# Kernel optimization log

Measured on AMD Instinct MI355X. Metric: run time of the kernel, lower is better.

## Reference

```python
import jax, jax.numpy as jnp
import numpy as np

T = 8192   # sequence length (= max_seq_len)
E = 1024   # embedding dim
D = 11     # hard-coded projection dim in source


def setup_inputs() -> dict:
    key = jax.random.key(0)
    ks = jax.random.split(key, 6)
    s_e = 1.0 / np.sqrt(E)
    s_d = 1.0 / np.sqrt(D)
    return {
        "x": jax.random.randint(ks[0], (T,), 0, 32000, dtype=jnp.int64),
        "x_embeddings": jax.random.normal(ks[1], (T, E), dtype=jnp.float32),
        "Wk": jax.random.normal(ks[2], (D, E), dtype=jnp.float32) * s_e,
        "bk": jnp.zeros((D,), dtype=jnp.float32),
        "Wq": jax.random.normal(ks[3], (D, E), dtype=jnp.float32) * s_e,
        "bq": jnp.zeros((D,), dtype=jnp.float32),
        "Wv": jax.random.normal(ks[4], (D, E), dtype=jnp.float32) * s_e,
        "bv": jnp.zeros((D,), dtype=jnp.float32),
        "Wf": jax.random.normal(ks[5], (E, D), dtype=jnp.float32) * s_d,
        "bf": jnp.zeros((E,), dtype=jnp.float32),
    }


def reference(x, x_embeddings, Wk, bk, Wq, bq, Wv, bv, Wf, bf):
    t = x.shape[0]  # static under jit
    k = x_embeddings @ Wk.T + bk            # [T, D]
    q = x_embeddings @ Wq.T + bq            # [T, D]
    v = x_embeddings @ Wv.T + bv            # [T, D]
    att = q @ k.T                           # [T, T]; NOTE: no 1/sqrt(D) scaling in source
    causal = jnp.tril(jnp.ones((t, t), dtype=bool))
    att = jnp.where(causal, att, -jnp.inf)
    att = jax.nn.softmax(att, axis=1)       # dim=1 as in source
    res = att @ v                           # [T, D]
    return res @ Wf.T + bf                  # [T, E]
```

## Files before the change

### kernel.cpp

```cpp
#include <hip/hip_runtime.h>

#define T_SEQ 8192
#define E_DIM 1024
#define QS 36
#define QNEC 16
#define QKC 64
#define QX4 16
#define QXST 17
#define QRB 64
#define AJC 64
#define ARB 128
#define KVW 24
#define NSLOT 128
#define TR 16

__device__ __forceinline__ float2 pkfma(float2 a, float2 b, float2 c) {
    return make_float2(fmaf(a.x, b.x, c.x), fmaf(a.y, b.y, c.y));
}
__device__ __forceinline__ float2 f2(float x, float y) { return make_float2(x, y); }


__global__ __launch_bounds__(256) void qkv_proj(
    const float* __restrict__ xe,
    const float* __restrict__ Wk, const float* __restrict__ bk,
    const float* __restrict__ Wq, const float* __restrict__ bq,
    const float* __restrict__ Wv, const float* __restrict__ bv,
    float* __restrict__ partQ) {
    const int row0 = blockIdx.x * QRB;
    const int ec = blockIdx.y;
    const int lane = threadIdx.x & 63;
    const int wg = threadIdx.x >> 6;
    const int cb = ec * QKC;

    __shared__ float4 xT[QRB * QXST];
    __shared__ float4 wT[36 * QX4];

#pragma unroll
    for (int t = 0; t < 4; ++t) {
        int idx = threadIdx.x + t * 256;
        int r = idx >> 4, c4 = idx & 15;
        xT[r * QXST + c4] =
            *(const float4*)(xe + (size_t)(row0 + r) * E_DIM + cb + c4 * 4);
    }
    for (int idx = threadIdx.x; idx < 36 * QX4; idx += 256) {
        int r = idx >> 4, c4 = idx & 15;
        float4 v = make_float4(0.f, 0.f, 0.f, 0.f);
        if (r < 33) {
            const float* base = (r < 11) ? (Wk + (size_t)r * E_DIM)
                              : (r < 22) ? (Wq + (size_t)(r - 11) * E_DIM)
                                         : (Wv + (size_t)(r - 22) * E_DIM);
            v = *(const float4*)(base + cb + c4 * 4);
        }
        wT[idx] = v;
    }
    __syncthreads();

    float2 acc[9];
#pragma unroll
    for (int k = 0; k < 9; ++k) acc[k] = f2(0.f, 0.f);

    const float4* xr = xT + lane * QXST;
    const float4* wr = wT + wg * 9 * QX4;
#pragma unroll 4
    for (int c4 = 0; c4 < QX4; ++c4) {
        float4 xv = xr[c4];
#pragma unroll
        for (int k = 0; k < 9; ++k) {
            float4 wv = wr[k * QX4 + c4];
            acc[k] = pkfma(f2(xv.x, xv.y), f2(wv.x, wv.y), acc[k]);
            acc[k] = pkfma(f2(xv.z, xv.w), f2(wv.z, wv.w), acc[k]);
        }
    }

    __syncthreads();
    float* res = (float*)xT;
#pragma unroll
    for (int k = 0; k < 9; ++k) {
        int o = wg * 9 + k;
        bool live = (o < 33);
        int c = (o < 11) ? o : (o < 22) ? o + 1 : (o < 33) ? o + 2
              : (o == 33) ? 11 : (o == 34) ? 23 : 35;
        float b = 0.f;
        if (ec == 0 && live)
            b = (o < 11) ? bk[o] : (o < 22) ? bq[o - 11] : bv[o - 22];
        res[lane * 36 + c] = live ? (acc[k].x + acc[k].y + b) : 0.f;
    }
    __syncthreads();

    float4* dst = (float4*)(partQ + ((size_t)ec * T_SEQ + row0) * QS);
    for (int idx = threadIdx.x; idx < QRB * 9; idx += 256) {
        int r = idx / 9, f = idx % 9;
        dst[idx] = *(const float4*)(res + r * 36 + f * 4);
    }
}

__global__ __launch_bounds__(256) void reduceQ(const float* __restrict__ partQ,
                                               float* __restrict__ qkvF) {
    const size_t idx = (size_t)blockIdx.x * 256 + threadIdx.x;
    const float4* p = (const float4*)partQ;
    const size_t cs = (size_t)T_SEQ * (QS / 4);
    float4 s = make_float4(0.f, 0.f, 0.f, 0.f);
#pragma unroll
    for (int c = 0; c < QNEC; ++c) {
        float4 a = p[idx + (size_t)c * cs];
        s.x += a.x; s.y += a.y; s.z += a.z; s.w += a.w;
    }
    ((float4*)qkvF)[idx] = s;
}

__global__ __launch_bounds__(128) void attn(const float* __restrict__ qkvF,
                                            float* __restrict__ part) {
    const int b = blockIdx.x;
    int rb = 0;
    while ((rb + 1) * (rb + 2) / 2 <= b) ++rb;
    const int p = b - rb * (rb + 1) / 2;
    const int lane = threadIdx.x & 63;
    const int wid = threadIdx.x >> 6;
    const int jc = 2 * p + wid;
    const int r0 = rb * ARB + lane * 2;
    const int j0 = jc * AJC;

    const float* qp0 = qkvF + (size_t)r0 * QS + 12;
    const float* qp1 = qp0 + QS;
    float2 qa[6], qb[6];
#pragma unroll
    for (int d = 0; d < 5; ++d) {
        qa[d] = f2(qp0[2 * d], qp0[2 * d + 1]);
        qb[d] = f2(qp1[2 * d], qp1[2 * d + 1]);
    }
    qa[5] = f2(qp0[10], 0.f);
    qb[5] = f2(qp1[10], 0.f);

    float2 oa[6], ob[6];
#pragma unroll
    for (int d = 0; d < 6; ++d) { oa[d] = f2(0.f, 0.f); ob[d] = f2(0.f, 0.f); }

    __shared__ float kvs[2][AJC * KVW];
    float* kv = kvs[wid];

#pragma unroll
    for (int t = 0; t < 6; ++t) {
        int idx = lane + t * 64;
        int row = idx / 6, f = idx % 6;
        int srcOff = f * 4 + (f >= 3 ? 12 : 0);
        float4 v = *(const float4*)(qkvF + (size_t)(j0 + row) * QS + srcOff);
        *(float4*)(kv + row * KVW + f * 4) = v;
    }
    __syncthreads();

    for (int jj = 0; jj < AJC; ++jj) {
        const float* kp = kv + jj * KVW;
        const float4 kA = *(const float4*)(kp);
        const float4 kB = *(const float4*)(kp + 4);
        const float4 kC = *(const float4*)(kp + 8);
        const float4 vA = *(const float4*)(kp + 12);
        const float4 vB = *(const float4*)(kp + 16);
        const float4 vC = *(const float4*)(kp + 20);
        const float2 k01 = f2(kA.x, kA.y), k23 = f2(kA.z, kA.w);
        const float2 k45 = f2(kB.x, kB.y), k67 = f2(kB.z, kB.w);
        const float2 k89 = f2(kC.x, kC.y), kXp = f2(kC.z, kC.w);

        float2 sa = pkfma(qa[0], k01, pkfma(qa[1], k23, pkfma(qa[2], k45,
                    pkfma(qa[3], k67, pkfma(qa[4], k89,
                    pkfma(qa[5], kXp, f2(0.f, 0.f)))))));
        float2 sb = pkfma(qb[0], k01, pkfma(qb[1], k23, pkfma(qb[2], k45,
                    pkfma(qb[3], k67, pkfma(qb[4], k89,
                    pkfma(qb[5], kXp, f2(0.f, 0.f)))))));
        float pa = __expf(sa.x + sa.y);
        float pb = __expf(sb.x + sb.y);
        const int j = j0 + jj;
        pa = (j <= r0)     ? pa : 0.f;
        pb = (j <= r0 + 1) ? pb : 0.f;
        float2 pa2 = f2(pa, pa), pb2 = f2(pb, pb);
        oa[0] = pkfma(pa2, f2(vA.x, vA.y), oa[0]);
        oa[1] = pkfma(pa2, f2(vA.z, vA.w), oa[1]);
        oa[2] = pkfma(pa2, f2(vB.x, vB.y), oa[2]);
        oa[3] = pkfma(pa2, f2(vB.z, vB.w), oa[3]);
        oa[4] = pkfma(pa2, f2(vC.x, vC.y), oa[4]);
        oa[5] = pkfma(pa2, f2(vC.z, 1.f),  oa[5]);
        ob[0] = pkfma(pb2, f2(vA.x, vA.y), ob[0]);
        ob[1] = pkfma(pb2, f2(vA.z, vA.w), ob[1]);
        ob[2] = pkfma(pb2, f2(vB.x, vB.y), ob[2]);
        ob[3] = pkfma(pb2, f2(vB.z, vB.w), ob[3]);
        ob[4] = pkfma(pb2, f2(vC.x, vC.y), ob[4]);
        ob[5] = pkfma(pb2, f2(vC.z, 1.f),  ob[5]);
    }

    float* d0 = part + ((size_t)jc * T_SEQ + r0) * 12;
    float4 t;
    t.x = oa[0].x; t.y = oa[0].y; t.z = oa[1].x; t.w = oa[1].y; *(float4*)(d0 + 0) = t;
    t.x = oa[2].x; t.y = oa[2].y; t.z = oa[3].x; t.w = oa[3].y; *(float4*)(d0 + 4) = t;
    t.x = oa[4].x; t.y = oa[4].y; t.z = oa[5].x; t.w = oa[5].y; *(float4*)(d0 + 8) = t;
    float* d1 = d0 + 12;
    t.x = ob[0].x; t.y = ob[0].y; t.z = ob[1].x; t.w = ob[1].y; *(float4*)(d1 + 0) = t;
    t.x = ob[2].x; t.y = ob[2].y; t.z = ob[3].x; t.w = ob[3].y; *(float4*)(d1 + 4) = t;
    t.x = ob[4].x; t.y = ob[4].y; t.z = ob[5].x; t.w = ob[5].y; *(float4*)(d1 + 8) = t;
}

__global__ __launch_bounds__(256) void pass2(const float* __restrict__ part,
                                             const float* __restrict__ Wf,
                                             const float* __restrict__ bf,
                                             float* __restrict__ out) {
    const int t0 = blockIdx.x * TR;
    __shared__ float res[TR][12];
    const int cnt = 2 * (t0 / ARB) + 2;
    if (threadIdx.x < TR * 12) {
        const float* p = part + (size_t)t0 * 12 + threadIdx.x;
        const size_t S = (size_t)T_SEQ * 12;
        float v[4];
#pragma unroll
        for (int u = 0; u < 4; ++u) v[u] = 0.f;
        int c = 0;
        for (; c + 4 <= cnt; c += 4) {
#pragma unroll
            for (int u = 0; u < 4; ++u) v[u] += p[(size_t)(c + u) * S];
        }
        for (; c < cnt; ++c) v[0] += p[(size_t)c * S];
        float sum = (v[0] + v[1]) + (v[2] + v[3]);
        const int d = threadIdx.x % 12;
        res[threadIdx.x / 12][d] = (d == 11) ? (1.f / sum) : sum;
    }
    __syncthreads();

    const int e0 = threadIdx.x * 4;
    float w[4][11];
    const float* wp = Wf + (size_t)e0 * 11;
#pragma unroll
    for (int ee = 0; ee < 4; ++ee)
#pragma unroll
        for (int i = 0; i < 11; ++i) w[ee][i] = wp[ee * 11 + i];
    const float4 bv = *(const float4*)(bf + e0);

    for (int r = 0; r < TR; ++r) {
        float rr[12];
#pragma unroll
        for (int d = 0; d < 12; ++d) rr[d] = res[r][d];
        float2 a0 = f2(0.f, 0.f), a1 = a0, a2 = a0, a3 = a0;
#pragma unroll
        for (int d = 0; d < 10; d += 2) {
            float2 rv = f2(rr[d], rr[d + 1]);
            a0 = pkfma(rv, f2(w[0][d], w[0][d + 1]), a0);
            a1 = pkfma(rv, f2(w[1][d], w[1][d + 1]), a1);
            a2 = pkfma(rv, f2(w[2][d], w[2][d + 1]), a2);
            a3 = pkfma(rv, f2(w[3][d], w[3][d + 1]), a3);
        }
        const float rl = rr[11];
        float4 ov;
        ov.x = (a0.x + a0.y + rr[10] * w[0][10]) * rl + bv.x;
        ov.y = (a1.x + a1.y + rr[10] * w[1][10]) * rl + bv.y;
        ov.z = (a2.x + a2.y + rr[10] * w[2][10]) * rl + bv.z;
        ov.w = (a3.x + a3.y + rr[10] * w[3][10]) * rl + bv.w;
        *(float4*)(out + (size_t)(t0 + r) * E_DIM + e0) = ov;
    }
}

extern "C" void kernel_launch(void* const* d_in, const int* in_sizes, int n_in,
                              void* d_out, int out_size, void* d_ws, size_t ws_size,
                              hipStream_t stream) {
    const float* xe = (const float*)d_in[1];
    const float* Wk = (const float*)d_in[2];
    const float* bk = (const float*)d_in[3];
    const float* Wq = (const float*)d_in[4];
    const float* bq = (const float*)d_in[5];
    const float* Wv = (const float*)d_in[6];
    const float* bv = (const float*)d_in[7];
    const float* Wf = (const float*)d_in[8];
    const float* bf = (const float*)d_in[9];
    float* out = (float*)d_out;

    float* qkvF  = (float*)d_ws;
    float* partQ = qkvF + (size_t)T_SEQ * QS;
    float* part  = partQ;

    qkv_proj<<<dim3(T_SEQ / QRB, QNEC), 256, 0, stream>>>(xe, Wk, bk, Wq, bq, Wv, bv, partQ);
    reduceQ<<<(T_SEQ * (QS / 4)) / 256, 256, 0, stream>>>(partQ, qkvF);
    const int nrb = T_SEQ / ARB;
    attn<<<nrb * (nrb + 1) / 2, 128, 0, stream>>>(qkvF, part);
    pass2<<<T_SEQ / TR, 256, 0, stream>>>(part, Wf, bf, out);
}
```

Baseline: 176.6 us.

## Raise attention register tile to four rows per lane and cut projection splits

The attention kernel now gives each lane four query rows instead of two, so every K/V row loaded from shared memory is reused across more rows. Row blocks double to 256 and the triangular block mapping is updated to match. The QKV projection loops over four E chunks per block, which cuts the split count from 16 to 4 and shrinks the partial-sum traffic that reduceQ reads. pass2 now reduces partials with 16 threads per row using float4 loads and a shared-memory tree. In exchange the attention kernel uses more registers and launches fewer, larger blocks.

```diff
diff --git a/kernel.cpp b/kernel.cpp
--- a/kernel.cpp
+++ b/kernel.cpp
@@ -3,13 +3,13 @@
 #define T_SEQ 8192
 #define E_DIM 1024
 #define QS 36
-#define QNEC 16
+#define QNEC 4
 #define QKC 64
 #define QX4 16
 #define QXST 17
 #define QRB 64
 #define AJC 64
-#define ARB 128
+#define ARB 256
 #define KVW 24
 #define NSLOT 128
 #define TR 16
@@ -30,45 +30,49 @@
     const int ec = blockIdx.y;
     const int lane = threadIdx.x & 63;
     const int wg = threadIdx.x >> 6;
-    const int cb = ec * QKC;
 
     __shared__ float4 xT[QRB * QXST];
     __shared__ float4 wT[36 * QX4];
 
-#pragma unroll
-    for (int t = 0; t < 4; ++t) {
-        int idx = threadIdx.x + t * 256;
-        int r = idx >> 4, c4 = idx & 15;
-        xT[r * QXST + c4] =
-            *(const float4*)(xe + (size_t)(row0 + r) * E_DIM + cb + c4 * 4);
-    }
-    for (int idx = threadIdx.x; idx < 36 * QX4; idx += 256) {
-        int r = idx >> 4, c4 = idx & 15;
-        float4 v = make_float4(0.f, 0.f, 0.f, 0.f);
-        if (r < 33) {
-            const float* base = (r < 11) ? (Wk + (size_t)r * E_DIM)
-                              : (r < 22) ? (Wq + (size_t)(r - 11) * E_DIM)
-                                         : (Wv + (size_t)(r - 22) * E_DIM);
-            v = *(const float4*)(base + cb + c4 * 4);
-        }
-        wT[idx] = v;
-    }
-    __syncthreads();
-
     float2 acc[9];
 #pragma unroll
     for (int k = 0; k < 9; ++k) acc[k] = f2(0.f, 0.f);
 
-    const float4* xr = xT + lane * QXST;
-    const float4* wr = wT + wg * 9 * QX4;
+    for (int cc = 0; cc < 4; ++cc) {
+        const int cb = ec * 256 + cc * QKC;
+        if (cc) __syncthreads();
+
+#pragma unroll
+        for (int t = 0; t < 4; ++t) {
+            int idx = threadIdx.x + t * 256;
+            int r = idx >> 4, c4 = idx & 15;
+            xT[r * QXST + c4] =
+                *(const float4*)(xe + (size_t)(row0 + r) * E_DIM + cb + c4 * 4);
+        }
+        for (int idx = threadIdx.x; idx < 36 * QX4; idx += 256) {
+            int r = idx >> 4, c4 = idx & 15;
+            float4 v = make_float4(0.f, 0.f, 0.f, 0.f);
+            if (r < 33) {
+                const float* base = (r < 11) ? (Wk + (size_t)r * E_DIM)
+                                  : (r < 22) ? (Wq + (size_t)(r - 11) * E_DIM)
+                                             : (Wv + (size_t)(r - 22) * E_DIM);
+                v = *(const float4*)(base + cb + c4 * 4);
+            }
+            wT[idx] = v;
+        }
+        __syncthreads();
+
+        const float4* xr = xT + lane * QXST;
+        const float4* wr = wT + wg * 9 * QX4;
 #pragma unroll 4
-    for (int c4 = 0; c4 < QX4; ++c4) {
-        float4 xv = xr[c4];
-#pragma unroll
-        for (int k = 0; k < 9; ++k) {
-            float4 wv = wr[k * QX4 + c4];
-            acc[k] = pkfma(f2(xv.x, xv.y), f2(wv.x, wv.y), acc[k]);
-            acc[k] = pkfma(f2(xv.z, xv.w), f2(wv.z, wv.w), acc[k]);
+        for (int c4 = 0; c4 < QX4; ++c4) {
+            float4 xv = xr[c4];
+#pragma unroll
+            for (int k = 0; k < 9; ++k) {
+                float4 wv = wr[k * QX4 + c4];
+                acc[k] = pkfma(f2(xv.x, xv.y), f2(wv.x, wv.y), acc[k]);
+                acc[k] = pkfma(f2(xv.z, xv.w), f2(wv.z, wv.w), acc[k]);
+            }
         }
     }
 
@@ -112,28 +116,24 @@
                                             float* __restrict__ part) {
     const int b = blockIdx.x;
     int rb = 0;
-    while ((rb + 1) * (rb + 2) / 2 <= b) ++rb;
-    const int p = b - rb * (rb + 1) / 2;
+    while ((rb + 1) * (rb + 2) <= b) ++rb;
+    const int p = b - rb * (rb + 1);
     const int lane = threadIdx.x & 63;
     const int wid = threadIdx.x >> 6;
     const int jc = 2 * p + wid;
-    const int r0 = rb * ARB + lane * 2;
+    const int r0 = rb * ARB + lane * 4;
     const int j0 = jc * AJC;
 
-    const float* qp0 = qkvF + (size_t)r0 * QS + 12;
-    const float* qp1 = qp0 + QS;
-    float2 qa[6], qb[6];
-#pragma unroll
-    for (int d = 0; d < 5; ++d) {
-        qa[d] = f2(qp0[2 * d], qp0[2 * d + 1]);
-        qb[d] = f2(qp1[2 * d], qp1[2 * d + 1]);
-    }
-    qa[5] = f2(qp0[10], 0.f);
-    qb[5] = f2(qp1[10], 0.f);
-
-    float2 oa[6], ob[6];
-#pragma unroll
-    for (int d = 0; d < 6; ++d) { oa[d] = f2(0.f, 0.f); ob[d] = f2(0.f, 0.f); }
+    float2 q[4][6], o[4][6];
+#pragma unroll
+    for (int i = 0; i < 4; ++i) {
+        const float* qp = qkvF + (size_t)(r0 + i) * QS + 12;
+#pragma unroll
+        for (int d = 0; d < 5; ++d) q[i][d] = f2(qp[2 * d], qp[2 * d + 1]);
+        q[i][5] = f2(qp[10], 0.f);
+#pragma unroll
+        for (int d = 0; d < 6; ++d) o[i][d] = f2(0.f, 0.f);
+    }
 
     __shared__ float kvs[2][AJC * KVW];
     float* kv = kvs[wid];
@@ -159,42 +159,36 @@
         const float2 k01 = f2(kA.x, kA.y), k23 = f2(kA.z, kA.w);
         const float2 k45 = f2(kB.x, kB.y), k67 = f2(kB.z, kB.w);
         const float2 k89 = f2(kC.x, kC.y), kXp = f2(kC.z, kC.w);
-
-        float2 sa = pkfma(qa[0], k01, pkfma(qa[1], k23, pkfma(qa[2], k45,
-                    pkfma(qa[3], k67, pkfma(qa[4], k89,
-                    pkfma(qa[5], kXp, f2(0.f, 0.f)))))));
-        float2 sb = pkfma(qb[0], k01, pkfma(qb[1], k23, pkfma(qb[2], k45,
-                    pkfma(qb[3], k67, pkfma(qb[4], k89,
-                    pkfma(qb[5], kXp, f2(0.f, 0.f)))))));
-        float pa = __expf(sa.x + sa.y);
-        float pb = __expf(sb.x + sb.y);
         const int j = j0 + jj;
-        pa = (j <= r0)     ? pa : 0.f;
-        pb = (j <= r0 + 1) ? pb : 0.f;
-        float2 pa2 = f2(pa, pa), pb2 = f2(pb, pb);
-        oa[0] = pkfma(pa2, f2(vA.x, vA.y), oa[0]);
-        oa[1] = pkfma(pa2, f2(vA.z, vA.w), oa[1]);
-        oa[2] = pkfma(pa2, f2(vB.x, vB.y), oa[2]);
-        oa[3] = pkfma(pa2, f2(vB.z, vB.w), oa[3]);
-        oa[4] = pkfma(pa2, f2(vC.x, vC.y), oa[4]);
-        oa[5] = pkfma(pa2, f2(vC.z, 1.f),  oa[5]);
-        ob[0] = pkfma(pb2, f2(vA.x, vA.y), ob[0]);
-        ob[1] = pkfma(pb2, f2(vA.z, vA.w), ob[1]);
-        ob[2] = pkfma(pb2, f2(vB.x, vB.y), ob[2]);
-        ob[3] = pkfma(pb2, f2(vB.z, vB.w), ob[3]);
-        ob[4] = pkfma(pb2, f2(vC.x, vC.y), ob[4]);
-        ob[5] = pkfma(pb2, f2(vC.z, 1.f),  ob[5]);
+
+#pragma unroll
+        for (int i = 0; i < 4; ++i) {
+            float2 s = pkfma(q[i][0], k01, pkfma(q[i][1], k23, pkfma(q[i][2], k45,
+                       pkfma(q[i][3], k67, pkfma(q[i][4], k89,
+                       pkfma(q[i][5], kXp, f2(0.f, 0.f)))))));
+            float pe = __expf(s.x + s.y);
+            pe = (j <= r0 + i) ? pe : 0.f;
+            float2 p2 = f2(pe, pe);
+            o[i][0] = pkfma(p2, f2(vA.x, vA.y), o[i][0]);
+            o[i][1] = pkfma(p2, f2(vA.z, vA.w), o[i][1]);
+            o[i][2] = pkfma(p2, f2(vB.x, vB.y), o[i][2]);
+            o[i][3] = pkfma(p2, f2(vB.z, vB.w), o[i][3]);
+            o[i][4] = pkfma(p2, f2(vC.x, vC.y), o[i][4]);
+            o[i][5] = pkfma(p2, f2(vC.z, 1.f),  o[i][5]);
+        }
     }
 
     float* d0 = part + ((size_t)jc * T_SEQ + r0) * 12;
-    float4 t;
-    t.x = oa[0].x; t.y = oa[0].y; t.z = oa[1].x; t.w = oa[1].y; *(float4*)(d0 + 0) = t;
-    t.x = oa[2].x; t.y = oa[2].y; t.z = oa[3].x; t.w = oa[3].y; *(float4*)(d0 + 4) = t;
-    t.x = oa[4].x; t.y = oa[4].y; t.z = oa[5].x; t.w = oa[5].y; *(float4*)(d0 + 8) = t;
-    float* d1 = d0 + 12;
-    t.x = ob[0].x; t.y = ob[0].y; t.z = ob[1].x; t.w = ob[1].y; *(float4*)(d1 + 0) = t;
-    t.x = ob[2].x; t.y = ob[2].y; t.z = ob[3].x; t.w = ob[3].y; *(float4*)(d1 + 4) = t;
-    t.x = ob[4].x; t.y = ob[4].y; t.z = ob[5].x; t.w = ob[5].y; *(float4*)(d1 + 8) = t;
+#pragma unroll
+    for (int i = 0; i < 4; ++i) {
+        float4 t;
+        t.x = o[i][0].x; t.y = o[i][0].y; t.z = o[i][1].x; t.w = o[i][1].y;
+        *(float4*)(d0 + i * 12 + 0) = t;
+        t.x = o[i][2].x; t.y = o[i][2].y; t.z = o[i][3].x; t.w = o[i][3].y;
+        *(float4*)(d0 + i * 12 + 4) = t;
+        t.x = o[i][4].x; t.y = o[i][4].y; t.z = o[i][5].x; t.w = o[i][5].y;
+        *(float4*)(d0 + i * 12 + 8) = t;
+    }
 }
 
 __global__ __launch_bounds__(256) void pass2(const float* __restrict__ part,
@@ -202,23 +196,34 @@
                                              const float* __restrict__ bf,
                                              float* __restrict__ out) {
     const int t0 = blockIdx.x * TR;
+    const int cnt = 4 * (t0 / ARB) + 4;
+    __shared__ float red[16][16][12];
     __shared__ float res[TR][12];
-    const int cnt = 2 * (t0 / ARB) + 2;
+    {
+        const int r = threadIdx.x >> 4;
+        const int s = threadIdx.x & 15;
+        float a[12];
+#pragma unroll
+        for (int d = 0; d < 12; ++d) a[d] = 0.f;
+        const size_t S = (size_t)T_SEQ * 12;
+        const float* p = part + (size_t)(t0 + r) * 12;
+        for (int c = s; c < cnt; c += 16) {
+            const float4* pc = (const float4*)(p + (size_t)c * S);
+            float4 x0 = pc[0], x1 = pc[1], x2 = pc[2];
+            a[0] += x0.x; a[1] += x0.y; a[2]  += x0.z; a[3]  += x0.w;
+            a[4] += x1.x; a[5] += x1.y; a[6]  += x1.z; a[7]  += x1.w;
+            a[8] += x2.x; a[9] += x2.y; a[10] += x2.z; a[11] += x2.w;
+        }
+#pragma unroll
+        for (int d = 0; d < 12; ++d) red[r][s][d] = a[d];
+    }
+    __syncthreads();
     if (threadIdx.x < TR * 12) {
-        const float* p = part + (size_t)t0 * 12 + threadIdx.x;
-        const size_t S = (size_t)T_SEQ * 12;
-        float v[4];
-#pragma unroll
-        for (int u = 0; u < 4; ++u) v[u] = 0.f;
-        int c = 0;
-        for (; c + 4 <= cnt; c += 4) {
-#pragma unroll
-            for (int u = 0; u < 4; ++u) v[u] += p[(size_t)(c + u) * S];
-        }
-        for (; c < cnt; ++c) v[0] += p[(size_t)c * S];
-        float sum = (v[0] + v[1]) + (v[2] + v[3]);
-        const int d = threadIdx.x % 12;
-        res[threadIdx.x / 12][d] = (d == 11) ? (1.f / sum) : sum;
+        const int r = threadIdx.x / 12, d = threadIdx.x % 12;
+        float sum = 0.f;
+#pragma unroll
+        for (int s = 0; s < 16; ++s) sum += red[r][s][d];
+        res[r][d] = (d == 11) ? (1.f / sum) : sum;
     }
     __syncthreads();
 
@@ -273,8 +278,8 @@
     float* part  = partQ;
 
     qkv_proj<<<dim3(T_SEQ / QRB, QNEC), 256, 0, stream>>>(xe, Wk, bk, Wq, bq, Wv, bv, partQ);
-    reduceQ<<<(T_SEQ * (QS / 4)) / 256, 256, 0, stream>>>(partQ, qkvF);
-    const int nrb = T_SEQ / ARB;
-    attn<<<nrb * (nrb + 1) / 2, 128, 0, stream>>>(qkvF, part);
+    reduceQ<<<(T_SEQ * QS / 4) / 256, 256, 0, stream>>>(partQ, qkvF);
+    const int nrg = T_SEQ / ARB;
+    attn<<<nrg * (nrg + 1), 128, 0, stream>>>(qkvF, part);
     pass2<<<T_SEQ / TR, 256, 0, stream>>>(part, Wf, bf, out);
 }
```

New measurement: 179.6 us. Within noise of the previous version (+1.7%).
